# Kernel optimization log

Hardware: AMD Instinct MI355X
Metric: run time of the kernel (lower is better)

## Reference

```python
import jax, jax.numpy as jnp
import numpy as np

K, N, M, D = 64, 8192, 8, 32  # locations, time steps, covariate features, memory depth


def setup_inputs() -> dict:
    key = jax.random.key(0)
    ks = jax.random.split(key, 6)
    obs = jax.random.uniform(ks[0], (K, N), dtype=jnp.float32)            # event counts [K, N]
    covs = jax.random.normal(ks[1], (K, N, M), dtype=jnp.float32)          # covariates  [K, N, M]
    hbeta = jnp.array([2.0], dtype=jnp.float32)                            # decay rate param (torch init: 2)
    halpha = jax.random.uniform(ks[2], (K, K), dtype=jnp.float32) * 0.01   # excitation matrix, U(0, 0.01)
    gamma = jax.random.uniform(ks[3], (K,), dtype=jnp.float32) * 0.01      # covariate gate, U(0, 0.01)
    W1 = jax.random.normal(ks[4], (20, 2 * D * M), dtype=jnp.float32) * 0.05
    b1 = jnp.zeros((20,), dtype=jnp.float32)
    W2 = jax.random.normal(ks[5], (1, 20), dtype=jnp.float32) * 0.05
    b2 = jnp.zeros((1,), dtype=jnp.float32)
    return dict(obs=obs, covs=covs, hbeta=hbeta, halpha=halpha, gamma=gamma,
                W1=W1, b1=b1, W2=W2, b2=b2)


def _forward(obs, covs, hbeta, halpha, gamma, W1, b1, W2, b2):
    k, n = obs.shape
    beta = hbeta[0]
    decay = jnp.exp(-beta)

    # Excitation: S[t] = sum_{tp < t} obs[:, tp] * beta * exp(-(t - tp) * beta)
    # exact O(N) linear recurrence instead of the original per-t O(t) resummation.
    def step(S, o):
        return decay * (S + beta * o), S
    _, S_all = jax.lax.scan(step, jnp.zeros((k,), obs.dtype), obs.T)  # [N, K]
    lam1 = jax.nn.softplus(jnp.einsum('kj,nj->kn', halpha, S_all))     # [K, N] (hmu = 0 in subclass)

    # Edge-padded covariate windows: window at t is padded[:, t : t + 2D, :]
    padded = jnp.concatenate([
        jnp.repeat(covs[:, :1, :], D, axis=1),   # left pad with first step
        covs,
        jnp.repeat(covs[:, -1:, :], D, axis=1),  # right pad with last step
    ], axis=1)                                   # [K, N + 2D, M]
    idx = jnp.arange(n)[:, None] + jnp.arange(2 * D)[None, :]  # [N, 2D]
    X = padded[:, idx, :].reshape(k, n, 2 * D * M)             # [K, N, 2DM], time-major then M (matches torch reshape)

    # Tiny 2-layer MLP with softplus activations, vectorized over (K, N)
    h = jax.nn.softplus(jnp.einsum('knf,hf->knh', X, W1) + b1)           # [K, N, 20]
    mu = jax.nn.softplus(jnp.einsum('knh,oh->kno', h, W2) + b2)[..., 0]  # [K, N]

    lams = lam1 + gamma[:, None] * mu                                    # [K, N]
    loglik = jnp.sum(obs * jnp.log(lams) - lams)
    return loglik, lams


def reference(obs, covs, hbeta, halpha, gamma, W1, b1, W2, b2):
    return _forward(obs, covs, hbeta, halpha, gamma, W1, b1, W2, b2)
```

## Files before the change

### kernel.cpp

```cpp
#include <hip/hip_runtime.h>
#include <hip/hip_bf16.h>
#include <math.h>

#define KL 64
#define NT 8192
#define MF 8
#define DD 32
#define WIN 64
#define HD 20
#define HP 32
#define KF 512
#define NB 256
#define NXB (NT / NB)
#define NBLK (NXB * KL)
#define NPART (NBLK * 4)
#define GRPS (KF / 8)
#define GROW 24
#define W1SZ (GRPS * GROW * 8)

typedef __attribute__((ext_vector_type(8))) short bf16x8;
typedef __attribute__((ext_vector_type(4))) float f32x4;

__device__ __forceinline__ float softplus_f(float x) {
    float e = __expf(-fabsf(x));
    return fmaxf(x, 0.0f) + __logf(1.0f + e);
}
__device__ __forceinline__ short f2bf(float x) {
    __hip_bfloat16 h = __float2bfloat16(x);
    return *reinterpret_cast<short*>(&h);
}

__global__ __launch_bounds__(256)
void pack_kernel(const float* __restrict__ W1, const float* __restrict__ b1,
                 const float* __restrict__ W2, short* __restrict__ W1b,
                 float* __restrict__ b1p, float* __restrict__ W2p) {
    int t = blockIdx.x * 256 + threadIdx.x;
    #pragma unroll
    for (int i = 0; i < 3; ++i) {
        int p = t + i * 4096;
        int e = p & 7;
        int rg = p >> 3;
        int r = rg % GROW;
        int grp = rg / GROW;
        W1b[p] = (r < HD) ? f2bf(W1[r * KF + grp * 8 + e]) : (short)0;
    }
    if (blockIdx.x == 0 && threadIdx.x < HP) {
        b1p[threadIdx.x] = (threadIdx.x < HD) ? b1[threadIdx.x] : 0.0f;
        W2p[threadIdx.x] = (threadIdx.x < HD) ? W2[threadIdx.x] : 0.0f;
    }
}

__global__ __launch_bounds__(256)
void mlp_mfma_kernel(const float* __restrict__ covs, const float* __restrict__ obs,
                     const float* __restrict__ halpha, const float* __restrict__ hbeta,
                     const short* __restrict__ W1b, const float* __restrict__ b1p,
                     const float* __restrict__ W2p, const float* __restrict__ b2,
                     const float* __restrict__ gamma, float* __restrict__ lams,
                     float* __restrict__ partial) {
    __shared__ short cov_s[4][128 * MF];
    __shared__ float T_s[4][128];
    __shared__ float hsum[4][64];

    int k    = blockIdx.y;
    int n0   = blockIdx.x * NB;
    int tid  = threadIdx.x;
    int lane = tid & 63;
    int wave = tid >> 6;
    int base = n0 + wave * 64;

    int n = base + lane;
    size_t idx = (size_t)k * NT + n;
    float obs_n = obs[idx];
    float beta  = hbeta[0];
    float gam   = gamma[k];
    float b2v   = b2[0];

    const float* cbase = covs + (size_t)k * NT * MF;
    {
        int t1 = base - DD + lane;
        t1 = t1 < 0 ? 0 : t1;
        int t2 = base + DD + lane;
        t2 = t2 > NT - 1 ? NT - 1 : t2;
        const float4* cp1 = (const float4*)(cbase + (size_t)t1 * MF);
        const float4* cp2 = (const float4*)(cbase + (size_t)t2 * MF);
        float4 a0 = cp1[0], a1 = cp1[1];
        float4 d0 = cp2[0], d1 = cp2[1];
        bf16x8 v1, v2;
        v1[0] = f2bf(a0.x); v1[1] = f2bf(a0.y); v1[2] = f2bf(a0.z); v1[3] = f2bf(a0.w);
        v1[4] = f2bf(a1.x); v1[5] = f2bf(a1.y); v1[6] = f2bf(a1.z); v1[7] = f2bf(a1.w);
        v2[0] = f2bf(d0.x); v2[1] = f2bf(d0.y); v2[2] = f2bf(d0.z); v2[3] = f2bf(d0.w);
        v2[4] = f2bf(d1.x); v2[5] = f2bf(d1.y); v2[6] = f2bf(d1.z); v2[7] = f2bf(d1.w);
        *(bf16x8*)&cov_s[wave][lane * MF] = v1;
        *(bf16x8*)&cov_s[wave][(lane + 64) * MF] = v2;
    }

    int c = lane & 15;
    int g = lane >> 4;

    f32x4 acc[4][2];
    #pragma unroll
    for (int mt = 0; mt < 4; ++mt) {
        acc[mt][0] = (f32x4){0.f, 0.f, 0.f, 0.f};
        acc[mt][1] = (f32x4){0.f, 0.f, 0.f, 0.f};
    }

    int r1 = (c < 4) ? (16 + c) : HD;
    const short* pB0 = W1b + g * (GROW * 8) + c * 8;
    const short* pB1 = W1b + g * (GROW * 8) + r1 * 8;
    const short* pA  = &cov_s[wave][(c + g) * MF];

    const float* arow = halpha + (size_t)k * KL;
    int tA = base - WIN + lane;
    tA = tA < 0 ? 0 : tA;
    int tB = base + lane;
    float aA = 0.0f, aB = 0.0f;

    #pragma unroll 2
    for (int kk = 0; kk < KF / 32; ++kk) {
        #pragma unroll
        for (int jj = 0; jj < 4; ++jj) {
            int j = kk * 4 + jj;
            float ajv = arow[j];
            const float* orow = obs + (size_t)j * NT;
            aA = fmaf(ajv, orow[tA], aA);
            aB = fmaf(ajv, orow[tB], aB);
        }
        bf16x8 b0  = *(const bf16x8*)(pB0 + kk * (4 * GROW * 8));
        bf16x8 b1v = *(const bf16x8*)(pB1 + kk * (4 * GROW * 8));
        #pragma unroll
        for (int mt = 0; mt < 4; ++mt) {
            bf16x8 a = *(const bf16x8*)(pA + (mt * 16 + kk * 4) * MF);
            acc[mt][0] = __builtin_amdgcn_mfma_f32_16x16x32_bf16(a, b0,  acc[mt][0], 0, 0, 0);
            acc[mt][1] = __builtin_amdgcn_mfma_f32_16x16x32_bf16(a, b1v, acc[mt][1], 0, 0, 0);
        }
    }
    T_s[wave][lane] = aA;
    T_s[wave][64 + lane] = aB;

    float w2a = W2p[c],      b1a = b1p[c];
    float w2b = W2p[16 + c], b1b = b1p[16 + c];
    float cur[16];
    #pragma unroll
    for (int mt = 0; mt < 4; ++mt) {
        #pragma unroll
        for (int j = 0; j < 4; ++j) {
            cur[mt * 4 + j] = w2a * softplus_f(acc[mt][0][j] + b1a)
                            + w2b * softplus_f(acc[mt][1][j] + b1b);
        }
    }
    #pragma unroll
    for (int m = 1; m <= 8; m <<= 1) {
        int half = 8 / m;
        #pragma unroll
        for (int s = 0; s < half; ++s) {
            float x0 = cur[s], x1 = cur[s + half];
            float t = (lane & m) ? x0 : x1;
            float u = __shfl_xor(t, m, 64);
            cur[s] = ((lane & m) ? x1 : x0) + u;
        }
    }
    {
        int iv = ((c & 1) << 3) | ((c & 2) << 1) | ((c & 4) >> 1) | ((c & 8) >> 3);
        hsum[wave][(iv >> 2) * 16 + g * 4 + (iv & 3)] = cur[0];
    }

    float decay = __expf(-beta);
    int Lmax = (int)(30.0f / beta) + 2;
    if (Lmax > WIN) Lmax = WIN;
    float la = 0.0f;
    const float* Tp = &T_s[wave][64 + lane];
    if (n >= WIN) {
        int it4 = (Lmax + 3) >> 2;
        float d2 = decay * decay;
        float d4 = d2 * d2;
        float w1 = beta * decay, w2 = w1 * decay, w3 = w2 * decay, w4 = w3 * decay;
        float la0 = 0.f, la1 = 0.f, la2 = 0.f, la3 = 0.f;
        for (int it = 0; it < it4; ++it) {
            int i = it * 4;
            la0 = fmaf(w1, Tp[-(i + 1)], la0); w1 *= d4;
            la1 = fmaf(w2, Tp[-(i + 2)], la1); w2 *= d4;
            la2 = fmaf(w3, Tp[-(i + 3)], la2); w3 *= d4;
            la3 = fmaf(w4, Tp[-(i + 4)], la3); w4 *= d4;
        }
        la = (la0 + la1) + (la2 + la3);
    } else {
        float w = beta * decay;
        for (int i = 1; i <= Lmax; ++i) {
            if (i <= n) la = fmaf(w, Tp[-i], la);
            w *= decay;
        }
    }
    float lam1 = softplus_f(la);
    float mu = softplus_f(hsum[wave][lane] + b2v);
    float lam = lam1 + gam * mu;
    lams[idx] = lam;
    float term = fmaf(obs_n, __logf(lam), -lam);

    #pragma unroll
    for (int off = 32; off > 0; off >>= 1) term += __shfl_down(term, off, 64);
    if (lane == 0)
        partial[((size_t)blockIdx.y * NXB + blockIdx.x) * 4 + wave] = term;
}

__global__ __launch_bounds__(256)
void finalize_kernel(const float* __restrict__ partial, float* __restrict__ out0) {
    __shared__ float wred[4];
    int tid = threadIdx.x;
    float s = 0.0f;
    #pragma unroll
    for (int i = 0; i < NPART / 256; ++i) s += partial[i * 256 + tid];
    #pragma unroll
    for (int off = 32; off > 0; off >>= 1) s += __shfl_down(s, off, 64);
    if ((tid & 63) == 0) wred[tid >> 6] = s;
    __syncthreads();
    if (tid == 0) out0[0] = (wred[0] + wred[1]) + (wred[2] + wred[3]);
}

extern "C" void kernel_launch(void* const* d_in, const int* in_sizes, int n_in,
                              void* d_out, int out_size, void* d_ws, size_t ws_size,
                              hipStream_t stream) {
    const float* obs    = (const float*)d_in[0];
    const float* covs   = (const float*)d_in[1];
    const float* hbeta  = (const float*)d_in[2];
    const float* halpha = (const float*)d_in[3];
    const float* gamma  = (const float*)d_in[4];
    const float* W1     = (const float*)d_in[5];
    const float* b1     = (const float*)d_in[6];
    const float* W2     = (const float*)d_in[7];
    const float* b2     = (const float*)d_in[8];

    float* out  = (float*)d_out;
    float* lams = out + 1;

    char* ws = (char*)d_ws;
    float* partial = (float*)ws;
    float* b1p     = (float*)(ws + 32768);
    float* W2p     = (float*)(ws + 32896);
    short* W1b     = (short*)(ws + 33024);

    dim3 block(256);
    pack_kernel<<<dim3(16), block, 0, stream>>>(W1, b1, W2, W1b, b1p, W2p);
    mlp_mfma_kernel<<<dim3(NXB, KL), block, 0, stream>>>(
        covs, obs, halpha, hbeta, W1b, b1p, W2p, b2, gamma, lams, partial);
    finalize_kernel<<<1, block, 0, stream>>>(partial, out);
}
```

Baseline: 43.22 us.

## Split GEMM and obs dot phases, stagger order across waves with setprio

The interleaved loop that mixed the 64-term halpha·obs dot product with the MFMA GEMM is split into two separate phases. Odd waves run the GEMM first and even waves run the dot product first, so memory-bound and MFMA-bound work from different waves can overlap on the same SIMD. The GEMM phase is wrapped in s_setprio to raise that wave's scheduling priority. The risk is losing the in-wave latency hiding that interleaving gave, plus some extra register pressure from the larger unroll.

```diff
diff --git a/kernel.cpp b/kernel.cpp
--- a/kernel.cpp
+++ b/kernel.cpp
@@ -49,6 +49,32 @@
         W2p[threadIdx.x] = (threadIdx.x < HD) ? W2[threadIdx.x] : 0.0f;
     }
 }
+
+#define TDOT_PHASE() do {                                                 \
+    _Pragma("unroll 16")                                                  \
+    for (int j = 0; j < KL; ++j) {                                        \
+        float ajv = arow[j];                                              \
+        const float* orow = obs + (size_t)j * NT;                         \
+        aA = fmaf(ajv, orow[tA], aA);                                     \
+        aB = fmaf(ajv, orow[tB], aB);                                     \
+    }                                                                     \
+} while (0)
+
+#define GEMM_PHASE() do {                                                 \
+    __builtin_amdgcn_s_setprio(1);                                        \
+    _Pragma("unroll 2")                                                   \
+    for (int kk = 0; kk < KF / 32; ++kk) {                                \
+        bf16x8 b0  = *(const bf16x8*)(pB0 + kk * (4 * GROW * 8));         \
+        bf16x8 b1v = *(const bf16x8*)(pB1 + kk * (4 * GROW * 8));         \
+        _Pragma("unroll")                                                 \
+        for (int mt = 0; mt < 4; ++mt) {                                  \
+            bf16x8 a = *(const bf16x8*)(pA + (mt * 16 + kk * 4) * MF);    \
+            acc[mt][0] = __builtin_amdgcn_mfma_f32_16x16x32_bf16(a, b0,  acc[mt][0], 0, 0, 0); \
+            acc[mt][1] = __builtin_amdgcn_mfma_f32_16x16x32_bf16(a, b1v, acc[mt][1], 0, 0, 0); \
+        }                                                                 \
+    }                                                                     \
+    __builtin_amdgcn_s_setprio(0);                                        \
+} while (0)
 
 __global__ __launch_bounds__(256)
 void mlp_mfma_kernel(const float* __restrict__ covs, const float* __restrict__ obs,
@@ -115,24 +141,12 @@
     int tB = base + lane;
     float aA = 0.0f, aB = 0.0f;
 
-    #pragma unroll 2
-    for (int kk = 0; kk < KF / 32; ++kk) {
-        #pragma unroll
-        for (int jj = 0; jj < 4; ++jj) {
-            int j = kk * 4 + jj;
-            float ajv = arow[j];
-            const float* orow = obs + (size_t)j * NT;
-            aA = fmaf(ajv, orow[tA], aA);
-            aB = fmaf(ajv, orow[tB], aB);
-        }
-        bf16x8 b0  = *(const bf16x8*)(pB0 + kk * (4 * GROW * 8));
-        bf16x8 b1v = *(const bf16x8*)(pB1 + kk * (4 * GROW * 8));
-        #pragma unroll
-        for (int mt = 0; mt < 4; ++mt) {
-            bf16x8 a = *(const bf16x8*)(pA + (mt * 16 + kk * 4) * MF);
-            acc[mt][0] = __builtin_amdgcn_mfma_f32_16x16x32_bf16(a, b0,  acc[mt][0], 0, 0, 0);
-            acc[mt][1] = __builtin_amdgcn_mfma_f32_16x16x32_bf16(a, b1v, acc[mt][1], 0, 0, 0);
-        }
+    if (wave & 1) {
+        GEMM_PHASE();
+        TDOT_PHASE();
+    } else {
+        TDOT_PHASE();
+        GEMM_PHASE();
     }
     T_s[wave][lane] = aA;
     T_s[wave][64 + lane] = aB;
```

Result: slower. 45.88 us (+6.2%).

## Share excitation prefix across 16-wave blocks and precompute decay weight table

Applied to the files above, without the earlier changes.

Blocks grow from 4 to 16 waves, and the per-block excitation values go into one shared array. Only the last wave computes the 64-step lookback halo, so the duplicated halpha·obs work is removed for all other waves, at the cost of a block-wide barrier. The decay weights are now precomputed in the pack kernel as a table, and a fast path runs a fixed 20-tap loop when beta is large enough. The code also uses packed bf16 conversion instructions and replaces the LDS transpose of the MLP output with a cross-lane shuffle.

```diff
diff --git a/kernel.cpp b/kernel.cpp
--- a/kernel.cpp
+++ b/kernel.cpp
@@ -10,16 +10,19 @@
 #define HD 20
 #define HP 32
 #define KF 512
-#define NB 256
-#define NXB (NT / NB)
-#define NBLK (NXB * KL)
-#define NPART (NBLK * 4)
+#define BS 1024
+#define WPB 16
+#define NCOLS (WPB * 64)
+#define GX (NT / NCOLS)
+#define NBLK (GX * KL)
+#define NPART (NBLK * WPB)
 #define GRPS (KF / 8)
 #define GROW 24
 #define W1SZ (GRPS * GROW * 8)
 
 typedef __attribute__((ext_vector_type(8))) short bf16x8;
 typedef __attribute__((ext_vector_type(4))) float f32x4;
+typedef __attribute__((ext_vector_type(4))) unsigned u32x4;
 
 __device__ __forceinline__ float softplus_f(float x) {
     float e = __expf(-fabsf(x));
@@ -29,11 +32,17 @@
     __hip_bfloat16 h = __float2bfloat16(x);
     return *reinterpret_cast<short*>(&h);
 }
+__device__ __forceinline__ unsigned pkbf(float a, float b) {
+    unsigned r;
+    asm("v_cvt_pk_bf16_f32 %0, %1, %2" : "=v"(r) : "v"(a), "v"(b));
+    return r;
+}
 
 __global__ __launch_bounds__(256)
 void pack_kernel(const float* __restrict__ W1, const float* __restrict__ b1,
-                 const float* __restrict__ W2, short* __restrict__ W1b,
-                 float* __restrict__ b1p, float* __restrict__ W2p) {
+                 const float* __restrict__ W2, const float* __restrict__ hbeta,
+                 short* __restrict__ W1b, float* __restrict__ b1p,
+                 float* __restrict__ W2p, float* __restrict__ wtab) {
     int t = blockIdx.x * 256 + threadIdx.x;
     #pragma unroll
     for (int i = 0; i < 3; ++i) {
@@ -48,25 +57,28 @@
         b1p[threadIdx.x] = (threadIdx.x < HD) ? b1[threadIdx.x] : 0.0f;
         W2p[threadIdx.x] = (threadIdx.x < HD) ? W2[threadIdx.x] : 0.0f;
     }
-}
-
-__global__ __launch_bounds__(256)
+    if (blockIdx.x == 0 && threadIdx.x < WIN) {
+        float bt = hbeta[0];
+        wtab[threadIdx.x] = bt * __expf(-bt * (float)(threadIdx.x + 1));
+    }
+}
+
+__global__ __launch_bounds__(BS)
 void mlp_mfma_kernel(const float* __restrict__ covs, const float* __restrict__ obs,
                      const float* __restrict__ halpha, const float* __restrict__ hbeta,
                      const short* __restrict__ W1b, const float* __restrict__ b1p,
                      const float* __restrict__ W2p, const float* __restrict__ b2,
-                     const float* __restrict__ gamma, float* __restrict__ lams,
-                     float* __restrict__ partial) {
-    __shared__ short cov_s[4][128 * MF];
-    __shared__ float T_s[4][128];
-    __shared__ float hsum[4][64];
+                     const float* __restrict__ gamma, const float* __restrict__ wt,
+                     float* __restrict__ lams, float* __restrict__ partial) {
+    __shared__ short cov_s[WPB][128 * MF];
+    __shared__ float T_s[NCOLS + WIN];
 
     int k    = blockIdx.y;
-    int n0   = blockIdx.x * NB;
+    int N0   = blockIdx.x * NCOLS;
     int tid  = threadIdx.x;
     int lane = tid & 63;
     int wave = tid >> 6;
-    int base = n0 + wave * 64;
+    int base = N0 + wave * 64;
 
     int n = base + lane;
     size_t idx = (size_t)k * NT + n;
@@ -85,13 +97,12 @@
         const float4* cp2 = (const float4*)(cbase + (size_t)t2 * MF);
         float4 a0 = cp1[0], a1 = cp1[1];
         float4 d0 = cp2[0], d1 = cp2[1];
-        bf16x8 v1, v2;
-        v1[0] = f2bf(a0.x); v1[1] = f2bf(a0.y); v1[2] = f2bf(a0.z); v1[3] = f2bf(a0.w);
-        v1[4] = f2bf(a1.x); v1[5] = f2bf(a1.y); v1[6] = f2bf(a1.z); v1[7] = f2bf(a1.w);
-        v2[0] = f2bf(d0.x); v2[1] = f2bf(d0.y); v2[2] = f2bf(d0.z); v2[3] = f2bf(d0.w);
-        v2[4] = f2bf(d1.x); v2[5] = f2bf(d1.y); v2[6] = f2bf(d1.z); v2[7] = f2bf(d1.w);
-        *(bf16x8*)&cov_s[wave][lane * MF] = v1;
-        *(bf16x8*)&cov_s[wave][(lane + 64) * MF] = v2;
+        u32x4 q1 = { pkbf(a0.x, a0.y), pkbf(a0.z, a0.w),
+                     pkbf(a1.x, a1.y), pkbf(a1.z, a1.w) };
+        u32x4 q2 = { pkbf(d0.x, d0.y), pkbf(d0.z, d0.w),
+                     pkbf(d1.x, d1.y), pkbf(d1.z, d1.w) };
+        *(u32x4*)&cov_s[wave][lane * MF] = q1;
+        *(u32x4*)&cov_s[wave][(lane + 64) * MF] = q2;
     }
 
     int c = lane & 15;
@@ -120,10 +131,14 @@
         #pragma unroll
         for (int jj = 0; jj < 4; ++jj) {
             int j = kk * 4 + jj;
-            float ajv = arow[j];
-            const float* orow = obs + (size_t)j * NT;
-            aA = fmaf(ajv, orow[tA], aA);
-            aB = fmaf(ajv, orow[tB], aB);
+            aA = fmaf(arow[j], (obs + (size_t)j * NT)[tA], aA);
+        }
+        if (wave == WPB - 1) {
+            #pragma unroll
+            for (int jj = 0; jj < 4; ++jj) {
+                int j = kk * 4 + jj;
+                aB = fmaf(arow[j], (obs + (size_t)j * NT)[tB], aB);
+            }
         }
         bf16x8 b0  = *(const bf16x8*)(pB0 + kk * (4 * GROW * 8));
         bf16x8 b1v = *(const bf16x8*)(pB1 + kk * (4 * GROW * 8));
@@ -134,8 +149,9 @@
             acc[mt][1] = __builtin_amdgcn_mfma_f32_16x16x32_bf16(a, b1v, acc[mt][1], 0, 0, 0);
         }
     }
-    T_s[wave][lane] = aA;
-    T_s[wave][64 + lane] = aB;
+    T_s[wave * 64 + lane] = aA;
+    if (wave == WPB - 1) T_s[NCOLS + lane] = aB;
+    __syncthreads();
 
     float w2a = W2p[c],      b1a = b1p[c];
     float w2b = W2p[16 + c], b1b = b1p[16 + c];
@@ -159,31 +175,31 @@
             cur[s] = ((lane & m) ? x1 : x0) + u;
         }
     }
+    float pre;
     {
-        int iv = ((c & 1) << 3) | ((c & 2) << 1) | ((c & 4) >> 1) | ((c & 8) >> 3);
-        hsum[wave][(iv >> 2) * 16 + g * 4 + (iv & 3)] = cur[0];
-    }
-
-    float decay = __expf(-beta);
-    int Lmax = (int)(30.0f / beta) + 2;
-    if (Lmax > WIN) Lmax = WIN;
+        int mt_ = lane >> 4, gg = (lane >> 2) & 3, jj_ = lane & 3;
+        int iv2 = (mt_ << 2) | jj_;
+        int src = gg * 16 + (((iv2 & 1) << 3) | ((iv2 & 2) << 1) |
+                             ((iv2 & 4) >> 1) | ((iv2 & 8) >> 3));
+        pre = __shfl(cur[0], src, 64);
+    }
+
+    const float* Tp = &T_s[64 + wave * 64 + lane];
     float la = 0.0f;
-    const float* Tp = &T_s[wave][64 + lane];
-    if (n >= WIN) {
-        int it4 = (Lmax + 3) >> 2;
-        float d2 = decay * decay;
-        float d4 = d2 * d2;
-        float w1 = beta * decay, w2 = w1 * decay, w3 = w2 * decay, w4 = w3 * decay;
+    if (base >= WIN && beta >= 1.6667f) {
         float la0 = 0.f, la1 = 0.f, la2 = 0.f, la3 = 0.f;
-        for (int it = 0; it < it4; ++it) {
-            int i = it * 4;
-            la0 = fmaf(w1, Tp[-(i + 1)], la0); w1 *= d4;
-            la1 = fmaf(w2, Tp[-(i + 2)], la1); w2 *= d4;
-            la2 = fmaf(w3, Tp[-(i + 3)], la2); w3 *= d4;
-            la3 = fmaf(w4, Tp[-(i + 4)], la3); w4 *= d4;
+        #pragma unroll
+        for (int it = 0; it < 5; ++it) {
+            la0 = fmaf(wt[4 * it + 0], Tp[-(4 * it + 1)], la0);
+            la1 = fmaf(wt[4 * it + 1], Tp[-(4 * it + 2)], la1);
+            la2 = fmaf(wt[4 * it + 2], Tp[-(4 * it + 3)], la2);
+            la3 = fmaf(wt[4 * it + 3], Tp[-(4 * it + 4)], la3);
         }
         la = (la0 + la1) + (la2 + la3);
     } else {
+        float decay = __expf(-beta);
+        int Lmax = (int)(30.0f / beta) + 2;
+        if (Lmax > WIN) Lmax = WIN;
         float w = beta * decay;
         for (int i = 1; i <= Lmax; ++i) {
             if (i <= n) la = fmaf(w, Tp[-i], la);
@@ -191,7 +207,7 @@
         }
     }
     float lam1 = softplus_f(la);
-    float mu = softplus_f(hsum[wave][lane] + b2v);
+    float mu = softplus_f(pre + b2v);
     float lam = lam1 + gam * mu;
     lams[idx] = lam;
     float term = fmaf(obs_n, __logf(lam), -lam);
@@ -199,7 +215,7 @@
     #pragma unroll
     for (int off = 32; off > 0; off >>= 1) term += __shfl_down(term, off, 64);
     if (lane == 0)
-        partial[((size_t)blockIdx.y * NXB + blockIdx.x) * 4 + wave] = term;
+        partial[((size_t)blockIdx.y * GX + blockIdx.x) * WPB + wave] = term;
 }
 
 __global__ __launch_bounds__(256)
@@ -236,11 +252,12 @@
     float* partial = (float*)ws;
     float* b1p     = (float*)(ws + 32768);
     float* W2p     = (float*)(ws + 32896);
-    short* W1b     = (short*)(ws + 33024);
-
-    dim3 block(256);
-    pack_kernel<<<dim3(16), block, 0, stream>>>(W1, b1, W2, W1b, b1p, W2p);
-    mlp_mfma_kernel<<<dim3(NXB, KL), block, 0, stream>>>(
-        covs, obs, halpha, hbeta, W1b, b1p, W2p, b2, gamma, lams, partial);
-    finalize_kernel<<<1, block, 0, stream>>>(partial, out);
-}
+    float* wtab    = (float*)(ws + 33024);
+    short* W1b     = (short*)(ws + 33280);
+
+    pack_kernel<<<dim3(16), dim3(256), 0, stream>>>(W1, b1, W2, hbeta,
+                                                    W1b, b1p, W2p, wtab);
+    mlp_mfma_kernel<<<dim3(GX, KL), dim3(BS), 0, stream>>>(
+        covs, obs, halpha, hbeta, W1b, b1p, W2p, b2, gamma, wtab, lams, partial);
+    finalize_kernel<<<1, dim3(256), 0, stream>>>(partial, out);
+}
```

New measurement: 43.45 us. About the same (+0.5%).
